# Kernel optimization log

Measured on AMD Instinct MI355X. Metric: run time of the kernel, lower is better.

## Reference

```python
import jax, jax.numpy as jnp
import numpy as np

N_NODES = 50000


def gcn_conv(x, W, b, src, dst, n_nodes):
    """GCNConv (PyG defaults): h = D^{-1/2}(A+I)D^{-1/2} (x @ W) + b, edge weights = 1.
    Self loops handled analytically (self-loop norm = 1/deg_i) to avoid growing edge arrays."""
    h = x @ W  # [N, out]
    # degree including self loop, computed on destination (col) per PyG gcn_norm
    deg = jax.ops.segment_sum(jnp.ones(src.shape[0], h.dtype), dst, num_segments=n_nodes) + 1.0
    dinv = jax.lax.rsqrt(deg)  # deg >= 1 so no clamping needed
    norm = dinv[src] * dinv[dst]  # [E]
    agg = jax.ops.segment_sum(h[src] * norm[:, None], dst, num_segments=n_nodes)
    agg = agg + h * (dinv * dinv)[:, None]  # self-loop contribution
    return agg + b


def setup_inputs() -> dict:
    key = jax.random.key(0)
    ks = jax.random.split(key, 6)
    n, e, d_in, d_hid = N_NODES, 800000, 128, 16
    x = jax.random.normal(ks[0], (n, d_in), dtype=jnp.float32)
    edge_index = jax.random.randint(ks[1], (2, e), 0, n, dtype=jnp.int64)
    W1 = jax.random.normal(ks[2], (d_in, d_hid), dtype=jnp.float32) * (1.0 / np.sqrt(d_in))
    b1 = jnp.zeros((d_hid,), jnp.float32)
    W2 = jax.random.normal(ks[3], (d_hid, d_in), dtype=jnp.float32) * (1.0 / np.sqrt(d_hid))
    b2 = jnp.zeros((d_in,), jnp.float32)
    return {"x": x, "edge_index": edge_index, "W1": W1, "b1": b1, "W2": W2, "b2": b2}


def reference(x, edge_index, W1, b1, W2, b2):
    src, dst = edge_index[0], edge_index[1]
    z = gcn_conv(x, W1, b1, src, dst, N_NODES)          # encoder: 128 -> 16
    recon = gcn_conv(z, W2, b2, src, dst, N_NODES)      # decoder: 16 -> 128
    return recon
```

## Files before the change

kernel.cpp:

```cpp
#include <hip/hip_runtime.h>


#define N_NODES 50000
#define N_EDGES 800000
#define D_IN    128
#define D_H     16
#define K_BUCK  512
#define NPB2    98
#define BSHIFT  11
#define BCAP    (1 << BSHIFT)
#define PA_BLKS 500
#define PA_CHUNK 1600
#define GC_PAD  16
#define G_BLKS  196
#define K4_NPB  128

__global__ __launch_bounds__(256) void k1_fused(
        const int* __restrict__ src, const int* __restrict__ dst,
        const float* __restrict__ x, const float* __restrict__ W1,
        int* __restrict__ gcur, float* __restrict__ h1, int* __restrict__ arr) {
    __shared__ __align__(16) float w1s[D_IN * D_H];
    __shared__ int hist[K_BUCK];
    __shared__ int cur[K_BUCK];
    int bid = blockIdx.x;
    int tid = threadIdx.x;

    if (bid < PA_BLKS) {
        int e0 = bid * PA_CHUNK;
        for (int b = tid; b < K_BUCK; b += 256) hist[b] = 0;
        __syncthreads();
        const int4* d4p = (const int4*)(dst + e0);
        const int4* s4p = (const int4*)(src + e0);
        for (int i = tid; i < PA_CHUNK / 4; i += 256) {
            int4 d = d4p[i];
            atomicAdd(&hist[d.x / NPB2], 1);
            atomicAdd(&hist[d.y / NPB2], 1);
            atomicAdd(&hist[d.z / NPB2], 1);
            atomicAdd(&hist[d.w / NPB2], 1);
        }
        __syncthreads();
        for (int b = tid; b < K_BUCK; b += 256)
            cur[b] = (b << BSHIFT) + atomicAdd(&gcur[b * GC_PAD], hist[b]);
        __syncthreads();
        for (int i = tid; i < PA_CHUNK / 4; i += 256) {
            int4 d = d4p[i];
            int4 s = s4p[i];
            int b0 = d.x / NPB2, b1 = d.y / NPB2, b2 = d.z / NPB2, b3 = d.w / NPB2;
            int p0 = atomicAdd(&cur[b0], 1);
            int p1 = atomicAdd(&cur[b1], 1);
            int p2 = atomicAdd(&cur[b2], 1);
            int p3 = atomicAdd(&cur[b3], 1);
            if (p0 < ((b0 + 1) << BSHIFT)) arr[p0] = (s.x << 7) | (d.x - b0 * NPB2);
            if (p1 < ((b1 + 1) << BSHIFT)) arr[p1] = (s.y << 7) | (d.y - b1 * NPB2);
            if (p2 < ((b2 + 1) << BSHIFT)) arr[p2] = (s.z << 7) | (d.z - b2 * NPB2);
            if (p3 < ((b3 + 1) << BSHIFT)) arr[p3] = (s.w << 7) | (d.w - b3 * NPB2);
        }
    } else {
        for (int i = tid; i < D_IN * D_H; i += 256) w1s[i] = W1[i];
        __syncthreads();
        int row = (bid - PA_BLKS) * 256 + tid;
        if (row >= N_NODES) return;
        const float4* xr = (const float4*)(x + row * D_IN);
        const float4* w4 = (const float4*)w1s;
        float4 a0 = {0, 0, 0, 0}, a1 = a0, a2 = a0, a3 = a0;
        for (int k4 = 0; k4 < D_IN / 4; ++k4) {
            float4 xv = xr[k4];
            #pragma unroll
            for (int j = 0; j < 4; ++j) {
                float xk = (j == 0) ? xv.x : (j == 1) ? xv.y : (j == 2) ? xv.z : xv.w;
                const float4* wr = w4 + (k4 * 4 + j) * 4;
                float4 w0 = wr[0], w1v = wr[1], w2v = wr[2], w3v = wr[3];
                a0.x += xk * w0.x;  a0.y += xk * w0.y;  a0.z += xk * w0.z;  a0.w += xk * w0.w;
                a1.x += xk * w1v.x; a1.y += xk * w1v.y; a1.z += xk * w1v.z; a1.w += xk * w1v.w;
                a2.x += xk * w2v.x; a2.y += xk * w2v.y; a2.z += xk * w2v.z; a2.w += xk * w2v.w;
                a3.x += xk * w3v.x; a3.y += xk * w3v.y; a3.z += xk * w3v.z; a3.w += xk * w3v.w;
            }
        }
        float4* hr = (float4*)(h1 + row * D_H);
        hr[0] = a0; hr[1] = a1; hr[2] = a2; hr[3] = a3;
    }
}

__global__ __launch_bounds__(256) void k2_build_csr(
        const int* __restrict__ arr, const int* __restrict__ gcur,
        float* __restrict__ h1, float* __restrict__ dinv,
        int* __restrict__ csr, int2* __restrict__ meta) {
    __shared__ int cnt[NPB2];
    __shared__ int pref[NPB2];
    __shared__ int cur[NPB2];
    __shared__ float sdi[NPB2];
    int k = blockIdx.x, tid = threadIdx.x;
    for (int i = tid; i < NPB2; i += 256) cnt[i] = 0;
    __syncthreads();
    int count = min(gcur[k * GC_PAD], BCAP);
    int base = k << BSHIFT;
    for (int i = tid; i < count; i += 256) atomicAdd(&cnt[arr[base + i] & 127], 1);
    __syncthreads();
    if (tid == 0) {
        int run = 0;
        for (int l = 0; l < NPB2; ++l) { pref[l] = run; run += cnt[l]; }
    }
    __syncthreads();
    int n0 = k * NPB2;
    int ncnt = min(NPB2, N_NODES - n0);
    for (int l = tid; l < ncnt; l += 256) {
        cur[l] = pref[l];
        meta[n0 + l] = make_int2(base + pref[l], cnt[l]);
        float di = rsqrtf((float)cnt[l] + 1.0f);
        sdi[l] = di;
        dinv[n0 + l] = di;
    }
    __syncthreads();
    for (int g = tid; g < ncnt * 4; g += 256) {
        int l = g >> 2;
        float di = sdi[l];
        float4* p = (float4*)(h1 + (n0 + l) * D_H);
        float4 v = p[g & 3];
        v.x *= di; v.y *= di; v.z *= di; v.w *= di;
        p[g & 3] = v;
    }
    for (int i = tid; i < count; i += 256) {
        int p = arr[base + i];
        int l = p & 127;
        int pos = atomicAdd(&cur[l], 1);
        csr[base + pos] = p >> 7;
    }
}

__global__ __launch_bounds__(256) void k3_agg_enc(
        const float4* __restrict__ h1s4, const int* __restrict__ csr,
        const int2* __restrict__ meta, const float* __restrict__ dinv,
        const float* __restrict__ b1, float4* __restrict__ zs4) {
    int tid = threadIdx.x;
    int q = tid & 3;
    int n = blockIdx.x * 64 + (tid >> 2);
    if (n >= N_NODES) return;
    int qb = tid & 60;
    int2 m = meta[n];
    int e = m.x, end = m.x + m.y;
    float4 acc = {0.0f, 0.0f, 0.0f, 0.0f};
    for (; e < end; e += 4) {
        int myidx = 0;
        if (e + q < end) myidx = csr[e + q];
        #pragma unroll
        for (int j = 0; j < 4; ++j) {
            int idx = __shfl(myidx, qb + j, 64);
            if (e + j < end) {
                float4 v = h1s4[idx * 4 + q];
                acc.x += v.x; acc.y += v.y; acc.z += v.z; acc.w += v.w;
            }
        }
    }
    float di = dinv[n];
    float4 hv = h1s4[n * 4 + q];
    float4 bv = ((const float4*)b1)[q];
    float4 z;
    z.x = di * (di * (acc.x + hv.x) + bv.x);
    z.y = di * (di * (acc.y + hv.y) + bv.y);
    z.z = di * (di * (acc.z + hv.z) + bv.z);
    z.w = di * (di * (acc.w + hv.w) + bv.w);
    zs4[n * 4 + q] = z;
}

__global__ __launch_bounds__(512) void k4_agg_dec_out(
        const float4* __restrict__ zs4, const int* __restrict__ csr,
        const int2* __restrict__ meta, const float* __restrict__ dinv,
        const float* __restrict__ W2, const float* __restrict__ b2,
        float* __restrict__ out) {
    __shared__ float agL[K4_NPB * 17];
    __shared__ __align__(16) float w2s[D_H * D_IN];
    int tid = threadIdx.x;
    for (int i = tid; i < D_H * D_IN; i += 512) w2s[i] = W2[i];
    int q = tid & 3;
    int nloc = tid >> 2;
    int n0 = blockIdx.x * K4_NPB;
    int n = n0 + nloc;
    int qb = tid & 60;
    if (n < N_NODES) {
        int2 m = meta[n];
        int e = m.x, end = m.x + m.y;
        float4 acc = {0.0f, 0.0f, 0.0f, 0.0f};
        for (; e < end; e += 4) {
            int myidx = 0;
            if (e + q < end) myidx = csr[e + q];
            #pragma unroll
            for (int j = 0; j < 4; ++j) {
                int idx = __shfl(myidx, qb + j, 64);
                if (e + j < end) {
                    float4 v = zs4[idx * 4 + q];
                    acc.x += v.x; acc.y += v.y; acc.z += v.z; acc.w += v.w;
                }
            }
        }
        float di = dinv[n];
        float4 zv = zs4[n * 4 + q];
        agL[nloc * 17 + q * 4 + 0] = di * (acc.x + zv.x);
        agL[nloc * 17 + q * 4 + 1] = di * (acc.y + zv.y);
        agL[nloc * 17 + q * 4 + 2] = di * (acc.z + zv.z);
        agL[nloc * 17 + q * 4 + 3] = di * (acc.w + zv.w);
    }
    __syncthreads();
    int quarter = tid >> 7;
    int ne = tid & 127;
    if (n0 + ne < N_NODES) {
        const float* arow = &agL[ne * 17];
        float4 o[8];
        const float4* b2q = (const float4*)(b2 + quarter * 32);
        #pragma unroll
        for (int u = 0; u < 8; ++u) o[u] = b2q[u];
        #pragma unroll
        for (int c = 0; c < D_H; ++c) {
            float ac = arow[c];
            const float4* wr = (const float4*)(w2s + c * D_IN + quarter * 32);
            #pragma unroll
            for (int u = 0; u < 8; ++u) {
                float4 w = wr[u];
                o[u].x += ac * w.x; o[u].y += ac * w.y;
                o[u].z += ac * w.z; o[u].w += ac * w.w;
            }
        }
        float4* orow = (float4*)(out + (n0 + ne) * D_IN + quarter * 32);
        #pragma unroll
        for (int u = 0; u < 8; ++u) orow[u] = o[u];
    }
}

extern "C" void kernel_launch(void* const* d_in, const int* in_sizes, int n_in,
                              void* d_out, int out_size, void* d_ws, size_t ws_size,
                              hipStream_t stream) {
    const float* x  = (const float*)d_in[0];
    const int*   ei = (const int*)d_in[1];
    const float* W1 = (const float*)d_in[2];
    const float* b1 = (const float*)d_in[3];
    const float* W2 = (const float*)d_in[4];
    const float* b2 = (const float*)d_in[5];
    float* out = (float*)d_out;

    const int* src = ei;
    const int* dst = ei + N_EDGES;

    char* base = (char*)d_ws;
    int*    gcur = (int*)base;                 base += K_BUCK * GC_PAD * 4;
    float*  dinv = (float*)base;               base += N_NODES * 4;
    float*  h1   = (float*)base;               base += N_NODES * D_H * 4;
    float*  zs   = (float*)base;               base += N_NODES * D_H * 4;
    int2*   meta = (int2*)base;                base += N_NODES * 8;
    int*    arr  = (int*)base;                 base += K_BUCK * BCAP * 4;
    int*    csr  = (int*)base;                 base += K_BUCK * BCAP * 4;

    hipMemsetAsync(gcur, 0, K_BUCK * GC_PAD * sizeof(int), stream);

    k1_fused<<<PA_BLKS + G_BLKS, 256, 0, stream>>>(src, dst, x, W1, gcur, h1, arr);
    k2_build_csr<<<K_BUCK, 256, 0, stream>>>(arr, gcur, h1, dinv, csr, meta);
    k3_agg_enc<<<(N_NODES + 63) / 64, 256, 0, stream>>>((const float4*)h1, csr, meta, dinv, b1, (float4*)zs);
    k4_agg_dec_out<<<(N_NODES + K4_NPB - 1) / K4_NPB, 512, 0, stream>>>((const float4*)zs, csr, meta, dinv, W2, b2, out);
}
```

Before: 162.0 us.

## Replace global atomic bucket cursors with per-block fixed-size bucket segments

The edge-partition phase no longer builds a per-block histogram and then reserves space with global atomics. Each partition block now scatters edges directly into its own 32-slot segment per destination bucket and writes per-bucket counts to a table, which also removes the workspace memset. The CSR build kernel then scans all 500 segments of its bucket, skipping slots beyond the stored counts. This drops a pass over the edges, the global atomics and the memset, but makes the intermediate array much larger and sparse, so the CSR build touches many mostly-empty cache lines. It also silently drops edges if any block puts more than 32 edges into one bucket.

After: 187.7 us. 15.9% more time.

```diff
diff --git a/kernel.cpp b/kernel.cpp
--- a/kernel.cpp
+++ b/kernel.cpp
@@ -11,54 +11,24 @@
 #define BCAP    (1 << BSHIFT)
 #define PA_BLKS 500
 #define PA_CHUNK 1600
-#define GC_PAD  16
+#define SEG     32
+#define SEG_SH  5
 #define G_BLKS  196
 #define K4_NPB  128
 
 __global__ __launch_bounds__(256) void k1_fused(
         const int* __restrict__ src, const int* __restrict__ dst,
         const float* __restrict__ x, const float* __restrict__ W1,
-        int* __restrict__ gcur, float* __restrict__ h1, int* __restrict__ arr) {
+        int* __restrict__ percnt, float* __restrict__ h1, int* __restrict__ arr) {
     __shared__ __align__(16) float w1s[D_IN * D_H];
-    __shared__ int hist[K_BUCK];
     __shared__ int cur[K_BUCK];
     int bid = blockIdx.x;
     int tid = threadIdx.x;
 
-    if (bid < PA_BLKS) {
-        int e0 = bid * PA_CHUNK;
-        for (int b = tid; b < K_BUCK; b += 256) hist[b] = 0;
-        __syncthreads();
-        const int4* d4p = (const int4*)(dst + e0);
-        const int4* s4p = (const int4*)(src + e0);
-        for (int i = tid; i < PA_CHUNK / 4; i += 256) {
-            int4 d = d4p[i];
-            atomicAdd(&hist[d.x / NPB2], 1);
-            atomicAdd(&hist[d.y / NPB2], 1);
-            atomicAdd(&hist[d.z / NPB2], 1);
-            atomicAdd(&hist[d.w / NPB2], 1);
-        }
-        __syncthreads();
-        for (int b = tid; b < K_BUCK; b += 256)
-            cur[b] = (b << BSHIFT) + atomicAdd(&gcur[b * GC_PAD], hist[b]);
-        __syncthreads();
-        for (int i = tid; i < PA_CHUNK / 4; i += 256) {
-            int4 d = d4p[i];
-            int4 s = s4p[i];
-            int b0 = d.x / NPB2, b1 = d.y / NPB2, b2 = d.z / NPB2, b3 = d.w / NPB2;
-            int p0 = atomicAdd(&cur[b0], 1);
-            int p1 = atomicAdd(&cur[b1], 1);
-            int p2 = atomicAdd(&cur[b2], 1);
-            int p3 = atomicAdd(&cur[b3], 1);
-            if (p0 < ((b0 + 1) << BSHIFT)) arr[p0] = (s.x << 7) | (d.x - b0 * NPB2);
-            if (p1 < ((b1 + 1) << BSHIFT)) arr[p1] = (s.y << 7) | (d.y - b1 * NPB2);
-            if (p2 < ((b2 + 1) << BSHIFT)) arr[p2] = (s.z << 7) | (d.z - b2 * NPB2);
-            if (p3 < ((b3 + 1) << BSHIFT)) arr[p3] = (s.w << 7) | (d.w - b3 * NPB2);
-        }
-    } else {
+    if (bid < G_BLKS) {
         for (int i = tid; i < D_IN * D_H; i += 256) w1s[i] = W1[i];
         __syncthreads();
-        int row = (bid - PA_BLKS) * 256 + tid;
+        int row = bid * 256 + tid;
         if (row >= N_NODES) return;
         const float4* xr = (const float4*)(x + row * D_IN);
         const float4* w4 = (const float4*)w1s;
@@ -78,23 +48,62 @@
         }
         float4* hr = (float4*)(h1 + row * D_H);
         hr[0] = a0; hr[1] = a1; hr[2] = a2; hr[3] = a3;
+    } else {
+        int blk = bid - G_BLKS;
+        int e0 = blk * PA_CHUNK;
+        for (int b = tid; b < K_BUCK; b += 256) cur[b] = 0;
+        __syncthreads();
+        const int4* d4p = (const int4*)(dst + e0);
+        const int4* s4p = (const int4*)(src + e0);
+        {
+            int4 d = d4p[tid];
+            int4 s = s4p[tid];
+            int k0 = d.x / NPB2, k1 = d.y / NPB2, k2 = d.z / NPB2, k3 = d.w / NPB2;
+            int p0 = atomicAdd(&cur[k0], 1);
+            int p1 = atomicAdd(&cur[k1], 1);
+            int p2 = atomicAdd(&cur[k2], 1);
+            int p3 = atomicAdd(&cur[k3], 1);
+            if (p0 < SEG) arr[(k0 * PA_BLKS + blk) * SEG + p0] = (s.x << 7) | (d.x - k0 * NPB2);
+            if (p1 < SEG) arr[(k1 * PA_BLKS + blk) * SEG + p1] = (s.y << 7) | (d.y - k1 * NPB2);
+            if (p2 < SEG) arr[(k2 * PA_BLKS + blk) * SEG + p2] = (s.z << 7) | (d.z - k2 * NPB2);
+            if (p3 < SEG) arr[(k3 * PA_BLKS + blk) * SEG + p3] = (s.w << 7) | (d.w - k3 * NPB2);
+        }
+        if (tid < PA_CHUNK / 4 - 256) {
+            int4 d = d4p[tid + 256];
+            int4 s = s4p[tid + 256];
+            int k0 = d.x / NPB2, k1 = d.y / NPB2, k2 = d.z / NPB2, k3 = d.w / NPB2;
+            int p0 = atomicAdd(&cur[k0], 1);
+            int p1 = atomicAdd(&cur[k1], 1);
+            int p2 = atomicAdd(&cur[k2], 1);
+            int p3 = atomicAdd(&cur[k3], 1);
+            if (p0 < SEG) arr[(k0 * PA_BLKS + blk) * SEG + p0] = (s.x << 7) | (d.x - k0 * NPB2);
+            if (p1 < SEG) arr[(k1 * PA_BLKS + blk) * SEG + p1] = (s.y << 7) | (d.y - k1 * NPB2);
+            if (p2 < SEG) arr[(k2 * PA_BLKS + blk) * SEG + p2] = (s.z << 7) | (d.z - k2 * NPB2);
+            if (p3 < SEG) arr[(k3 * PA_BLKS + blk) * SEG + p3] = (s.w << 7) | (d.w - k3 * NPB2);
+        }
+        __syncthreads();
+        for (int b = tid; b < K_BUCK; b += 256) percnt[blk * K_BUCK + b] = cur[b];
     }
 }
 
 __global__ __launch_bounds__(256) void k2_build_csr(
-        const int* __restrict__ arr, const int* __restrict__ gcur,
+        const int* __restrict__ arr, const int* __restrict__ percnt,
         float* __restrict__ h1, float* __restrict__ dinv,
         int* __restrict__ csr, int2* __restrict__ meta) {
     __shared__ int cnt[NPB2];
     __shared__ int pref[NPB2];
-    __shared__ int cur[NPB2];
+    __shared__ int curL[NPB2];
     __shared__ float sdi[NPB2];
+    __shared__ int c500[PA_BLKS];
     int k = blockIdx.x, tid = threadIdx.x;
     for (int i = tid; i < NPB2; i += 256) cnt[i] = 0;
-    __syncthreads();
-    int count = min(gcur[k * GC_PAD], BCAP);
-    int base = k << BSHIFT;
-    for (int i = tid; i < count; i += 256) atomicAdd(&cnt[arr[base + i] & 127], 1);
+    for (int b = tid; b < PA_BLKS; b += 256) c500[b] = min(percnt[b * K_BUCK + k], SEG);
+    __syncthreads();
+    const int* __restrict__ ab = arr + k * (PA_BLKS * SEG);
+    for (int s = tid; s < PA_BLKS * SEG; s += 256) {
+        if ((s & (SEG - 1)) < c500[s >> SEG_SH])
+            atomicAdd(&cnt[ab[s] & 127], 1);
+    }
     __syncthreads();
     if (tid == 0) {
         int run = 0;
@@ -103,8 +112,9 @@
     __syncthreads();
     int n0 = k * NPB2;
     int ncnt = min(NPB2, N_NODES - n0);
+    int base = k << BSHIFT;
     for (int l = tid; l < ncnt; l += 256) {
-        cur[l] = pref[l];
+        curL[l] = pref[l];
         meta[n0 + l] = make_int2(base + pref[l], cnt[l]);
         float di = rsqrtf((float)cnt[l] + 1.0f);
         sdi[l] = di;
@@ -119,11 +129,13 @@
         v.x *= di; v.y *= di; v.z *= di; v.w *= di;
         p[g & 3] = v;
     }
-    for (int i = tid; i < count; i += 256) {
-        int p = arr[base + i];
-        int l = p & 127;
-        int pos = atomicAdd(&cur[l], 1);
-        csr[base + pos] = p >> 7;
+    for (int s = tid; s < PA_BLKS * SEG; s += 256) {
+        if ((s & (SEG - 1)) < c500[s >> SEG_SH]) {
+            int p = ab[s];
+            int l = p & 127;
+            int pos = atomicAdd(&curL[l], 1);
+            if (pos < BCAP) csr[base + pos] = p >> 7;
+        }
     }
 }
 
@@ -240,18 +252,16 @@
     const int* dst = ei + N_EDGES;
 
     char* base = (char*)d_ws;
-    int*    gcur = (int*)base;                 base += K_BUCK * GC_PAD * 4;
-    float*  dinv = (float*)base;               base += N_NODES * 4;
-    float*  h1   = (float*)base;               base += N_NODES * D_H * 4;
-    float*  zs   = (float*)base;               base += N_NODES * D_H * 4;
-    int2*   meta = (int2*)base;                base += N_NODES * 8;
-    int*    arr  = (int*)base;                 base += K_BUCK * BCAP * 4;
-    int*    csr  = (int*)base;                 base += K_BUCK * BCAP * 4;
-
-    hipMemsetAsync(gcur, 0, K_BUCK * GC_PAD * sizeof(int), stream);
-
-    k1_fused<<<PA_BLKS + G_BLKS, 256, 0, stream>>>(src, dst, x, W1, gcur, h1, arr);
-    k2_build_csr<<<K_BUCK, 256, 0, stream>>>(arr, gcur, h1, dinv, csr, meta);
+    int*    percnt = (int*)base;               base += PA_BLKS * K_BUCK * 4;
+    float*  dinv   = (float*)base;             base += N_NODES * 4;
+    float*  h1     = (float*)base;             base += N_NODES * D_H * 4;
+    float*  zs     = (float*)base;             base += N_NODES * D_H * 4;
+    int2*   meta   = (int2*)base;              base += N_NODES * 8;
+    int*    arr    = (int*)base;               base += (size_t)K_BUCK * PA_BLKS * SEG * 4;
+    int*    csr    = (int*)base;               base += K_BUCK * BCAP * 4;
+
+    k1_fused<<<G_BLKS + PA_BLKS, 256, 0, stream>>>(src, dst, x, W1, percnt, h1, arr);
+    k2_build_csr<<<K_BUCK, 256, 0, stream>>>(arr, percnt, h1, dinv, csr, meta);
     k3_agg_enc<<<(N_NODES + 63) / 64, 256, 0, stream>>>((const float4*)h1, csr, meta, dinv, b1, (float4*)zs);
     k4_agg_dec_out<<<(N_NODES + K4_NPB - 1) / K4_NPB, 512, 0, stream>>>((const float4*)zs, csr, meta, dinv, W2, b2, out);
 }
```

## Fuse all GCN stages into one persistent kernel with grid-wide barriers

Applied to the files above, without the earlier changes.

Replaces the memset plus four kernel launches with a small init kernel and a single persistent 512-block kernel. The stages (GEMM plus bucket scatter, CSR build, encoder aggregation, decoder aggregation plus output GEMM) are separated by software grid barriers built on atomic counters. This removes launch gaps and inter-kernel drains, and the scatter phase now keeps the packed destination values in registers between the histogram and scatter passes. The cost is spin-wait barrier overhead, fewer blocks per phase, and a deadlock risk if all 512 blocks cannot be co-resident.

Result: slower. 567.2 us (+250.2%).

```diff
diff --git a/kernel.cpp b/kernel.cpp
--- a/kernel.cpp
+++ b/kernel.cpp
@@ -9,219 +9,269 @@
 #define NPB2    98
 #define BSHIFT  11
 #define BCAP    (1 << BSHIFT)
-#define PA_BLKS 500
-#define PA_CHUNK 1600
 #define GC_PAD  16
-#define G_BLKS  196
-#define K4_NPB  128
-
-__global__ __launch_bounds__(256) void k1_fused(
+#define GRID    512
+#define NTHR    256
+#define GEMM_BLKS 196
+#define SC_BLKS 316
+#define SC_CH   2536
+#define SC_I4   634
+#define NBLK3   782
+#define NBLK4   391
+#define BAR_PAD 16
+#define NBAR    3
+
+union SMem {
+    float w1s[D_IN * D_H];
+    struct { int hist[K_BUCK]; int cur[K_BUCK]; } s;
+    struct { int cnt[NPB2]; int pref[NPB2]; int cur[NPB2]; float sdi[NPB2]; } p2;
+    struct { float agL[128 * 17]; float w2s[D_H * D_IN]; } p4;
+};
+
+__global__ __launch_bounds__(256) void k_init(int* __restrict__ gcur,
+                                              int* __restrict__ bc) {
+    int t = blockIdx.x * 256 + threadIdx.x;
+    if (t < K_BUCK * GC_PAD) gcur[t] = 0;
+    if (t < NBAR * 8 * BAR_PAD) bc[t] = 0;
+}
+
+__device__ __forceinline__ void gbar(int* bc, int phase) {
+    __syncthreads();
+    if (threadIdx.x == 0) {
+        int* base = bc + phase * 8 * BAR_PAD;
+        __threadfence();
+        __hip_atomic_fetch_add(base + (blockIdx.x & 7) * BAR_PAD, 1,
+                               __ATOMIC_RELEASE, __HIP_MEMORY_SCOPE_AGENT);
+        int s;
+        do {
+            s = 0;
+            #pragma unroll
+            for (int j = 0; j < 8; ++j)
+                s += __hip_atomic_load(base + j * BAR_PAD,
+                                       __ATOMIC_ACQUIRE, __HIP_MEMORY_SCOPE_AGENT);
+            if (s < GRID) __builtin_amdgcn_s_sleep(2);
+        } while (s < GRID);
+    }
+    __syncthreads();
+}
+
+#define PACKH(pk, d) { \
+    int c0 = d.x / NPB2, c1 = d.y / NPB2, c2 = d.z / NPB2, c3 = d.w / NPB2; \
+    pk.x = (c0 << 7) | (d.x - c0 * NPB2); pk.y = (c1 << 7) | (d.y - c1 * NPB2); \
+    pk.z = (c2 << 7) | (d.z - c2 * NPB2); pk.w = (c3 << 7) | (d.w - c3 * NPB2); \
+    atomicAdd(&sm.s.hist[c0], 1); atomicAdd(&sm.s.hist[c1], 1); \
+    atomicAdd(&sm.s.hist[c2], 1); atomicAdd(&sm.s.hist[c3], 1); }
+
+#define SCAT(pk, sv) { \
+    int c0 = pk.x >> 7, c1 = pk.y >> 7, c2 = pk.z >> 7, c3 = pk.w >> 7; \
+    int q0 = atomicAdd(&sm.s.cur[c0], 1); int q1 = atomicAdd(&sm.s.cur[c1], 1); \
+    int q2 = atomicAdd(&sm.s.cur[c2], 1); int q3 = atomicAdd(&sm.s.cur[c3], 1); \
+    if (q0 < ((c0 + 1) << BSHIFT)) arr[q0] = (sv.x << 7) | (pk.x & 127); \
+    if (q1 < ((c1 + 1) << BSHIFT)) arr[q1] = (sv.y << 7) | (pk.y & 127); \
+    if (q2 < ((c2 + 1) << BSHIFT)) arr[q2] = (sv.z << 7) | (pk.z & 127); \
+    if (q3 < ((c3 + 1) << BSHIFT)) arr[q3] = (sv.w << 7) | (pk.w & 127); }
+
+__global__ __launch_bounds__(NTHR) void mega(
         const int* __restrict__ src, const int* __restrict__ dst,
         const float* __restrict__ x, const float* __restrict__ W1,
-        int* __restrict__ gcur, float* __restrict__ h1, int* __restrict__ arr) {
-    __shared__ __align__(16) float w1s[D_IN * D_H];
-    __shared__ int hist[K_BUCK];
-    __shared__ int cur[K_BUCK];
-    int bid = blockIdx.x;
-    int tid = threadIdx.x;
-
-    if (bid < PA_BLKS) {
-        int e0 = bid * PA_CHUNK;
-        for (int b = tid; b < K_BUCK; b += 256) hist[b] = 0;
-        __syncthreads();
-        const int4* d4p = (const int4*)(dst + e0);
-        const int4* s4p = (const int4*)(src + e0);
-        for (int i = tid; i < PA_CHUNK / 4; i += 256) {
-            int4 d = d4p[i];
-            atomicAdd(&hist[d.x / NPB2], 1);
-            atomicAdd(&hist[d.y / NPB2], 1);
-            atomicAdd(&hist[d.z / NPB2], 1);
-            atomicAdd(&hist[d.w / NPB2], 1);
-        }
-        __syncthreads();
-        for (int b = tid; b < K_BUCK; b += 256)
-            cur[b] = (b << BSHIFT) + atomicAdd(&gcur[b * GC_PAD], hist[b]);
-        __syncthreads();
-        for (int i = tid; i < PA_CHUNK / 4; i += 256) {
-            int4 d = d4p[i];
-            int4 s = s4p[i];
-            int b0 = d.x / NPB2, b1 = d.y / NPB2, b2 = d.z / NPB2, b3 = d.w / NPB2;
-            int p0 = atomicAdd(&cur[b0], 1);
-            int p1 = atomicAdd(&cur[b1], 1);
-            int p2 = atomicAdd(&cur[b2], 1);
-            int p3 = atomicAdd(&cur[b3], 1);
-            if (p0 < ((b0 + 1) << BSHIFT)) arr[p0] = (s.x << 7) | (d.x - b0 * NPB2);
-            if (p1 < ((b1 + 1) << BSHIFT)) arr[p1] = (s.y << 7) | (d.y - b1 * NPB2);
-            if (p2 < ((b2 + 1) << BSHIFT)) arr[p2] = (s.z << 7) | (d.z - b2 * NPB2);
-            if (p3 < ((b3 + 1) << BSHIFT)) arr[p3] = (s.w << 7) | (d.w - b3 * NPB2);
-        }
-    } else {
-        for (int i = tid; i < D_IN * D_H; i += 256) w1s[i] = W1[i];
-        __syncthreads();
-        int row = (bid - PA_BLKS) * 256 + tid;
-        if (row >= N_NODES) return;
-        const float4* xr = (const float4*)(x + row * D_IN);
-        const float4* w4 = (const float4*)w1s;
-        float4 a0 = {0, 0, 0, 0}, a1 = a0, a2 = a0, a3 = a0;
-        for (int k4 = 0; k4 < D_IN / 4; ++k4) {
-            float4 xv = xr[k4];
-            #pragma unroll
-            for (int j = 0; j < 4; ++j) {
-                float xk = (j == 0) ? xv.x : (j == 1) ? xv.y : (j == 2) ? xv.z : xv.w;
-                const float4* wr = w4 + (k4 * 4 + j) * 4;
-                float4 w0 = wr[0], w1v = wr[1], w2v = wr[2], w3v = wr[3];
-                a0.x += xk * w0.x;  a0.y += xk * w0.y;  a0.z += xk * w0.z;  a0.w += xk * w0.w;
-                a1.x += xk * w1v.x; a1.y += xk * w1v.y; a1.z += xk * w1v.z; a1.w += xk * w1v.w;
-                a2.x += xk * w2v.x; a2.y += xk * w2v.y; a2.z += xk * w2v.z; a2.w += xk * w2v.w;
-                a3.x += xk * w3v.x; a3.y += xk * w3v.y; a3.z += xk * w3v.z; a3.w += xk * w3v.w;
-            }
-        }
-        float4* hr = (float4*)(h1 + row * D_H);
-        hr[0] = a0; hr[1] = a1; hr[2] = a2; hr[3] = a3;
-    }
-}
-
-__global__ __launch_bounds__(256) void k2_build_csr(
-        const int* __restrict__ arr, const int* __restrict__ gcur,
-        float* __restrict__ h1, float* __restrict__ dinv,
-        int* __restrict__ csr, int2* __restrict__ meta) {
-    __shared__ int cnt[NPB2];
-    __shared__ int pref[NPB2];
-    __shared__ int cur[NPB2];
-    __shared__ float sdi[NPB2];
-    int k = blockIdx.x, tid = threadIdx.x;
-    for (int i = tid; i < NPB2; i += 256) cnt[i] = 0;
-    __syncthreads();
-    int count = min(gcur[k * GC_PAD], BCAP);
-    int base = k << BSHIFT;
-    for (int i = tid; i < count; i += 256) atomicAdd(&cnt[arr[base + i] & 127], 1);
-    __syncthreads();
-    if (tid == 0) {
-        int run = 0;
-        for (int l = 0; l < NPB2; ++l) { pref[l] = run; run += cnt[l]; }
-    }
-    __syncthreads();
-    int n0 = k * NPB2;
-    int ncnt = min(NPB2, N_NODES - n0);
-    for (int l = tid; l < ncnt; l += 256) {
-        cur[l] = pref[l];
-        meta[n0 + l] = make_int2(base + pref[l], cnt[l]);
-        float di = rsqrtf((float)cnt[l] + 1.0f);
-        sdi[l] = di;
-        dinv[n0 + l] = di;
-    }
-    __syncthreads();
-    for (int g = tid; g < ncnt * 4; g += 256) {
-        int l = g >> 2;
-        float di = sdi[l];
-        float4* p = (float4*)(h1 + (n0 + l) * D_H);
-        float4 v = p[g & 3];
-        v.x *= di; v.y *= di; v.z *= di; v.w *= di;
-        p[g & 3] = v;
-    }
-    for (int i = tid; i < count; i += 256) {
-        int p = arr[base + i];
-        int l = p & 127;
-        int pos = atomicAdd(&cur[l], 1);
-        csr[base + pos] = p >> 7;
-    }
-}
-
-__global__ __launch_bounds__(256) void k3_agg_enc(
-        const float4* __restrict__ h1s4, const int* __restrict__ csr,
-        const int2* __restrict__ meta, const float* __restrict__ dinv,
-        const float* __restrict__ b1, float4* __restrict__ zs4) {
-    int tid = threadIdx.x;
-    int q = tid & 3;
-    int n = blockIdx.x * 64 + (tid >> 2);
-    if (n >= N_NODES) return;
-    int qb = tid & 60;
-    int2 m = meta[n];
-    int e = m.x, end = m.x + m.y;
-    float4 acc = {0.0f, 0.0f, 0.0f, 0.0f};
-    for (; e < end; e += 4) {
-        int myidx = 0;
-        if (e + q < end) myidx = csr[e + q];
-        #pragma unroll
-        for (int j = 0; j < 4; ++j) {
-            int idx = __shfl(myidx, qb + j, 64);
-            if (e + j < end) {
-                float4 v = h1s4[idx * 4 + q];
-                acc.x += v.x; acc.y += v.y; acc.z += v.z; acc.w += v.w;
-            }
-        }
-    }
-    float di = dinv[n];
-    float4 hv = h1s4[n * 4 + q];
-    float4 bv = ((const float4*)b1)[q];
-    float4 z;
-    z.x = di * (di * (acc.x + hv.x) + bv.x);
-    z.y = di * (di * (acc.y + hv.y) + bv.y);
-    z.z = di * (di * (acc.z + hv.z) + bv.z);
-    z.w = di * (di * (acc.w + hv.w) + bv.w);
-    zs4[n * 4 + q] = z;
-}
-
-__global__ __launch_bounds__(512) void k4_agg_dec_out(
-        const float4* __restrict__ zs4, const int* __restrict__ csr,
-        const int2* __restrict__ meta, const float* __restrict__ dinv,
-        const float* __restrict__ W2, const float* __restrict__ b2,
-        float* __restrict__ out) {
-    __shared__ float agL[K4_NPB * 17];
-    __shared__ __align__(16) float w2s[D_H * D_IN];
-    int tid = threadIdx.x;
-    for (int i = tid; i < D_H * D_IN; i += 512) w2s[i] = W2[i];
-    int q = tid & 3;
-    int nloc = tid >> 2;
-    int n0 = blockIdx.x * K4_NPB;
-    int n = n0 + nloc;
-    int qb = tid & 60;
-    if (n < N_NODES) {
-        int2 m = meta[n];
-        int e = m.x, end = m.x + m.y;
-        float4 acc = {0.0f, 0.0f, 0.0f, 0.0f};
-        for (; e < end; e += 4) {
-            int myidx = 0;
-            if (e + q < end) myidx = csr[e + q];
-            #pragma unroll
-            for (int j = 0; j < 4; ++j) {
-                int idx = __shfl(myidx, qb + j, 64);
-                if (e + j < end) {
-                    float4 v = zs4[idx * 4 + q];
-                    acc.x += v.x; acc.y += v.y; acc.z += v.z; acc.w += v.w;
+        const float* __restrict__ b1, const float* __restrict__ W2,
+        const float* __restrict__ b2,
+        int* __restrict__ gcur, int* __restrict__ bc, float* __restrict__ dinv,
+        float* __restrict__ h1, float* __restrict__ zs,
+        int2* __restrict__ meta, int* __restrict__ arr,
+        int* __restrict__ csr, float* __restrict__ out) {
+    __shared__ __align__(16) SMem sm;
+    int bid = blockIdx.x, tid = threadIdx.x;
+
+    if (bid < GEMM_BLKS) {
+        for (int i = tid; i < D_IN * D_H; i += NTHR) sm.w1s[i] = W1[i];
+        __syncthreads();
+        int row = bid * NTHR + tid;
+        if (row < N_NODES) {
+            const float4* xr = (const float4*)(x + row * D_IN);
+            const float4* w4 = (const float4*)sm.w1s;
+            float4 a0 = {0, 0, 0, 0}, a1 = a0, a2 = a0, a3 = a0;
+            for (int k4 = 0; k4 < D_IN / 4; ++k4) {
+                float4 xv = xr[k4];
+                #pragma unroll
+                for (int j = 0; j < 4; ++j) {
+                    float xk = (j == 0) ? xv.x : (j == 1) ? xv.y : (j == 2) ? xv.z : xv.w;
+                    const float4* wr = w4 + (k4 * 4 + j) * 4;
+                    float4 w0 = wr[0], w1v = wr[1], w2v = wr[2], w3v = wr[3];
+                    a0.x += xk * w0.x;  a0.y += xk * w0.y;  a0.z += xk * w0.z;  a0.w += xk * w0.w;
+                    a1.x += xk * w1v.x; a1.y += xk * w1v.y; a1.z += xk * w1v.z; a1.w += xk * w1v.w;
+                    a2.x += xk * w2v.x; a2.y += xk * w2v.y; a2.z += xk * w2v.z; a2.w += xk * w2v.w;
+                    a3.x += xk * w3v.x; a3.y += xk * w3v.y; a3.z += xk * w3v.z; a3.w += xk * w3v.w;
                 }
             }
-        }
-        float di = dinv[n];
-        float4 zv = zs4[n * 4 + q];
-        agL[nloc * 17 + q * 4 + 0] = di * (acc.x + zv.x);
-        agL[nloc * 17 + q * 4 + 1] = di * (acc.y + zv.y);
-        agL[nloc * 17 + q * 4 + 2] = di * (acc.z + zv.z);
-        agL[nloc * 17 + q * 4 + 3] = di * (acc.w + zv.w);
-    }
-    __syncthreads();
-    int quarter = tid >> 7;
-    int ne = tid & 127;
-    if (n0 + ne < N_NODES) {
-        const float* arow = &agL[ne * 17];
-        float4 o[8];
-        const float4* b2q = (const float4*)(b2 + quarter * 32);
+            float4* hr = (float4*)(h1 + row * D_H);
+            hr[0] = a0; hr[1] = a1; hr[2] = a2; hr[3] = a3;
+        }
+    } else {
+        int base_e = (bid - GEMM_BLKS) * SC_CH;
+        int ni4 = min((N_EDGES - base_e) >> 2, SC_I4);
+        for (int b = tid; b < K_BUCK; b += NTHR) sm.s.hist[b] = 0;
+        __syncthreads();
+        const int4* d4p = (const int4*)(dst + base_e);
+        const int4* s4p = (const int4*)(src + base_e);
+        int4 pk0, pk1, pk2;
+        bool a0 = tid < ni4, a1 = tid + 256 < ni4, a2 = tid + 512 < ni4;
+        if (a0) { int4 d = d4p[tid];       PACKH(pk0, d); }
+        if (a1) { int4 d = d4p[tid + 256]; PACKH(pk1, d); }
+        if (a2) { int4 d = d4p[tid + 512]; PACKH(pk2, d); }
+        __syncthreads();
+        for (int b = tid; b < K_BUCK; b += NTHR)
+            sm.s.cur[b] = (b << BSHIFT) + atomicAdd(&gcur[b * GC_PAD], sm.s.hist[b]);
+        __syncthreads();
+        if (a0) { int4 sv = s4p[tid];       SCAT(pk0, sv); }
+        if (a1) { int4 sv = s4p[tid + 256]; SCAT(pk1, sv); }
+        if (a2) { int4 sv = s4p[tid + 512]; SCAT(pk2, sv); }
+    }
+    gbar(bc, 0);
+
+    {
+        int k = bid;
+        for (int i = tid; i < NPB2; i += NTHR) sm.p2.cnt[i] = 0;
+        __syncthreads();
+        int count = min(gcur[k * GC_PAD], BCAP);
+        int base = k << BSHIFT;
+        for (int i = tid; i < count; i += NTHR) atomicAdd(&sm.p2.cnt[arr[base + i] & 127], 1);
+        __syncthreads();
+        if (tid == 0) {
+            int run = 0;
+            for (int l = 0; l < NPB2; ++l) { sm.p2.pref[l] = run; run += sm.p2.cnt[l]; }
+        }
+        __syncthreads();
+        int n0 = k * NPB2;
+        int ncnt = min(NPB2, N_NODES - n0);
+        for (int l = tid; l < ncnt; l += NTHR) {
+            sm.p2.cur[l] = sm.p2.pref[l];
+            meta[n0 + l] = make_int2(base + sm.p2.pref[l], sm.p2.cnt[l]);
+            float di = rsqrtf((float)sm.p2.cnt[l] + 1.0f);
+            sm.p2.sdi[l] = di;
+            dinv[n0 + l] = di;
+        }
+        __syncthreads();
+        for (int g = tid; g < ncnt * 4; g += NTHR) {
+            int l = g >> 2;
+            float di = sm.p2.sdi[l];
+            float4* p = (float4*)(h1 + (n0 + l) * D_H);
+            float4 v = p[g & 3];
+            v.x *= di; v.y *= di; v.z *= di; v.w *= di;
+            p[g & 3] = v;
+        }
+        for (int i = tid; i < count; i += NTHR) {
+            int p = arr[base + i];
+            int l = p & 127;
+            int pos = atomicAdd(&sm.p2.cur[l], 1);
+            csr[base + pos] = p >> 7;
+        }
+    }
+    gbar(bc, 1);
+
+    {
+        const float4* h1s4 = (const float4*)h1;
+        float4* zs4 = (float4*)zs;
+        int q = tid & 3, qb = tid & 60;
         #pragma unroll
-        for (int u = 0; u < 8; ++u) o[u] = b2q[u];
-        #pragma unroll
-        for (int c = 0; c < D_H; ++c) {
-            float ac = arow[c];
-            const float4* wr = (const float4*)(w2s + c * D_IN + quarter * 32);
+        for (int pass = 0; pass < 2; ++pass) {
+            int vb = bid + pass * GRID;
+            int n = vb * 64 + (tid >> 2);
+            if (vb < NBLK3 && n < N_NODES) {
+                int2 m = meta[n];
+                int e = m.x, end = m.x + m.y;
+                float4 acc = {0.0f, 0.0f, 0.0f, 0.0f};
+                for (; e < end; e += 4) {
+                    int myidx = 0;
+                    if (e + q < end) myidx = csr[e + q];
+                    #pragma unroll
+                    for (int j = 0; j < 4; ++j) {
+                        int idx = __shfl(myidx, qb + j, 64);
+                        if (e + j < end) {
+                            float4 v = h1s4[idx * 4 + q];
+                            acc.x += v.x; acc.y += v.y; acc.z += v.z; acc.w += v.w;
+                        }
+                    }
+                }
+                float di = dinv[n];
+                float4 hv = h1s4[n * 4 + q];
+                float4 bv = ((const float4*)b1)[q];
+                float4 z;
+                z.x = di * (di * (acc.x + hv.x) + bv.x);
+                z.y = di * (di * (acc.y + hv.y) + bv.y);
+                z.z = di * (di * (acc.z + hv.z) + bv.z);
+                z.w = di * (di * (acc.w + hv.w) + bv.w);
+                zs4[n * 4 + q] = z;
+            }
+        }
+    }
+    gbar(bc, 2);
+
+    {
+        const float4* zs4 = (const float4*)zs;
+        for (int i = tid; i < D_H * D_IN; i += NTHR) sm.p4.w2s[i] = W2[i];
+        int q = tid & 3, qb = tid & 60;
+        bool blkact = (bid < NBLK4);
+        int n0b = bid * 128;
+        if (blkact) {
             #pragma unroll
-            for (int u = 0; u < 8; ++u) {
-                float4 w = wr[u];
-                o[u].x += ac * w.x; o[u].y += ac * w.y;
-                o[u].z += ac * w.z; o[u].w += ac * w.w;
+            for (int pass = 0; pass < 2; ++pass) {
+                int nloc = pass * 64 + (tid >> 2);
+                int n = n0b + nloc;
+                if (n < N_NODES) {
+                    int2 m = meta[n];
+                    int e = m.x, end = m.x + m.y;
+                    float4 acc = {0.0f, 0.0f, 0.0f, 0.0f};
+                    for (; e < end; e += 4) {
+                        int myidx = 0;
+                        if (e + q < end) myidx = csr[e + q];
+                        #pragma unroll
+                        for (int j = 0; j < 4; ++j) {
+                            int idx = __shfl(myidx, qb + j, 64);
+                            if (e + j < end) {
+                                float4 v = zs4[idx * 4 + q];
+                                acc.x += v.x; acc.y += v.y; acc.z += v.z; acc.w += v.w;
+                            }
+                        }
+                    }
+                    float di = dinv[n];
+                    float4 zv = zs4[n * 4 + q];
+                    sm.p4.agL[nloc * 17 + q * 4 + 0] = di * (acc.x + zv.x);
+                    sm.p4.agL[nloc * 17 + q * 4 + 1] = di * (acc.y + zv.y);
+                    sm.p4.agL[nloc * 17 + q * 4 + 2] = di * (acc.z + zv.z);
+                    sm.p4.agL[nloc * 17 + q * 4 + 3] = di * (acc.w + zv.w);
+                }
             }
         }
-        float4* orow = (float4*)(out + (n0 + ne) * D_IN + quarter * 32);
-        #pragma unroll
-        for (int u = 0; u < 8; ++u) orow[u] = o[u];
+        __syncthreads();
+        if (blkact) {
+            #pragma unroll
+            for (int pass = 0; pass < 2; ++pass) {
+                int quarter = pass * 2 + (tid >> 7);
+                int ne = tid & 127;
+                if (n0b + ne < N_NODES) {
+                    const float* arow = &sm.p4.agL[ne * 17];
+                    float4 o[8];
+                    const float4* b2q = (const float4*)(b2 + quarter * 32);
+                    #pragma unroll
+                    for (int u = 0; u < 8; ++u) o[u] = b2q[u];
+                    #pragma unroll
+                    for (int c = 0; c < D_H; ++c) {
+                        float ac = arow[c];
+                        const float4* wr = (const float4*)(sm.p4.w2s + c * D_IN + quarter * 32);
+                        #pragma unroll
+                        for (int u = 0; u < 8; ++u) {
+                            float4 w = wr[u];
+                            o[u].x += ac * w.x; o[u].y += ac * w.y;
+                            o[u].z += ac * w.z; o[u].w += ac * w.w;
+                        }
+                    }
+                    float4* orow = (float4*)(out + (n0b + ne) * D_IN + quarter * 32);
+                    #pragma unroll
+                    for (int u = 0; u < 8; ++u) orow[u] = o[u];
+                }
+            }
+        }
     }
 }
 
@@ -241,6 +291,7 @@
 
     char* base = (char*)d_ws;
     int*    gcur = (int*)base;                 base += K_BUCK * GC_PAD * 4;
+    int*    bc   = (int*)base;                 base += NBAR * 8 * BAR_PAD * 4;
     float*  dinv = (float*)base;               base += N_NODES * 4;
     float*  h1   = (float*)base;               base += N_NODES * D_H * 4;
     float*  zs   = (float*)base;               base += N_NODES * D_H * 4;
@@ -248,10 +299,7 @@
     int*    arr  = (int*)base;                 base += K_BUCK * BCAP * 4;
     int*    csr  = (int*)base;                 base += K_BUCK * BCAP * 4;
 
-    hipMemsetAsync(gcur, 0, K_BUCK * GC_PAD * sizeof(int), stream);
-
-    k1_fused<<<PA_BLKS + G_BLKS, 256, 0, stream>>>(src, dst, x, W1, gcur, h1, arr);
-    k2_build_csr<<<K_BUCK, 256, 0, stream>>>(arr, gcur, h1, dinv, csr, meta);
-    k3_agg_enc<<<(N_NODES + 63) / 64, 256, 0, stream>>>((const float4*)h1, csr, meta, dinv, b1, (float4*)zs);
-    k4_agg_dec_out<<<(N_NODES + K4_NPB - 1) / K4_NPB, 512, 0, stream>>>((const float4*)zs, csr, meta, dinv, W2, b2, out);
+    k_init<<<(K_BUCK * GC_PAD + 255) / 256, 256, 0, stream>>>(gcur, bc);
+    mega<<<GRID, NTHR, 0, stream>>>(src, dst, x, W1, b1, W2, b2,
+                                    gcur, bc, dinv, h1, zs, meta, arr, csr, out);
 }
```
